# Kernel tuning notes

Measured on AMD Instinct MI355X. Metric: run time of the kernel, lower is better.

Reference implementation:

```python
import jax, jax.numpy as jnp
import numpy as np

B, D, H, W = 16, 96, 96, 96
NUM_POINTS = 4096
THRESH = 0.5
CH = [3, 64, 128, 256, 512]   # shared-MLP channel progression (3 mlp layers + global_dim)
GROUPS = 8
EPS = 1e-5
HEAD_HIDDEN = 128


def setup_inputs() -> dict:
    key = jax.random.key(0)
    ks = jax.random.split(key, 8)
    inp = {"volume": jax.random.uniform(ks[0], (B, 1, D, H, W), jnp.float32)}
    for i in range(4):
        # Conv1d(kernel=1, no bias) weight (out, in); kaiming normal fan_out -> std=sqrt(2/out)
        inp[f"w{i+1}"] = jax.random.normal(ks[1 + i], (CH[i + 1], CH[i]), jnp.float32) * np.sqrt(2.0 / CH[i + 1]).astype(np.float32)
        inp[f"gn{i+1}_w"] = jnp.ones((CH[i + 1],), jnp.float32)
        inp[f"gn{i+1}_b"] = jnp.zeros((CH[i + 1],), jnp.float32)
    inp["fc1_w"] = jax.random.normal(ks[5], (HEAD_HIDDEN, CH[-1]), jnp.float32) * np.sqrt(2.0 / HEAD_HIDDEN).astype(np.float32)
    inp["fc1_b"] = jnp.zeros((HEAD_HIDDEN,), jnp.float32)
    inp["fc2_w"] = jax.random.normal(ks[6], (1, HEAD_HIDDEN), jnp.float32) * np.sqrt(2.0).astype(np.float32)
    inp["fc2_b"] = jnp.zeros((1,), jnp.float32)
    return inp


def volume_to_points(volume):
    """Batched, jit-safe version of volume_to_pointcloud (eval mode: linspace sampling)."""
    b, _, d, h, w = volume.shape
    mask = (volume[:, 0] > THRESH).reshape(b, -1)              # (B, D*H*W)
    n = mask.sum(axis=1)                                        # (B,) foreground counts
    # Stable argsort on ~mask puts foreground flat-indices first, in ascending order
    # == torch nonzero() ordering (row-major over D,H,W).
    order = jnp.argsort(jnp.logical_not(mask), axis=1, stable=True)  # (B, D*H*W)
    p = jnp.arange(NUM_POINTS)
    n_f = n.astype(jnp.float32)[:, None]
    # torch.linspace(0, n-1, P).long(): truncation toward zero
    lin = (p[None, :].astype(jnp.float32) * (n_f - 1.0) / (NUM_POINTS - 1)).astype(jnp.int32)
    lin = jnp.clip(lin, 0, jnp.maximum(n[:, None] - 1, 0))
    wrap = p[None, :] % jnp.maximum(n[:, None], 1)              # n < P fallback
    idx = jnp.where(n[:, None] >= NUM_POINTS, lin, wrap)        # (B, P)
    flat = jnp.take_along_axis(order, idx, axis=1)              # (B, P) flat voxel indices
    dd = flat // (h * w)
    hh = (flat // w) % h
    ww = flat % w
    coords = jnp.stack([dd, hh, ww], axis=1).astype(jnp.float32)  # (B, 3, P)
    scale = jnp.array([max(d - 1, 1), max(h - 1, 1), max(w - 1, 1)], jnp.float32)
    pts = coords / scale[None, :, None] * 2.0 - 1.0
    return jnp.where((n > 0)[:, None, None], pts, 0.0)


def group_norm(x, gamma, beta):
    b, c, npts = x.shape
    xg = x.reshape(b, GROUPS, c // GROUPS, npts)
    mu = xg.mean(axis=(2, 3), keepdims=True)
    var = xg.var(axis=(2, 3), keepdims=True)
    xn = ((xg - mu) * jax.lax.rsqrt(var + EPS)).reshape(b, c, npts)
    return xn * gamma[None, :, None] + beta[None, :, None]


def reference(volume, w1, gn1_w, gn1_b, w2, gn2_w, gn2_b, w3, gn3_w, gn3_b,
              w4, gn4_w, gn4_b, fc1_w, fc1_b, fc2_w, fc2_b):
    x = volume_to_points(volume)                                 # (B, 3, P)
    for cw, gw, gb in ((w1, gn1_w, gn1_b), (w2, gn2_w, gn2_b),
                       (w3, gn3_w, gn3_b), (w4, gn4_w, gn4_b)):
        x = jax.nn.relu(group_norm(jnp.einsum('oc,bcn->bon', cw, x), gw, gb))
    g = x.max(axis=2)                                            # (B, 512) global max-pool
    hdn = jax.nn.relu(g @ fc1_w.T + fc1_b)                       # dropout is identity in eval
    logits = (hdn @ fc2_w.T + fc2_b)[:, 0]                       # squeeze(-1) -> (B,)
    return logits
```

## Files before the change

kernel.cpp:

```cpp
#include <hip/hip_runtime.h>
#include <hip/hip_bf16.h>

#define NB 16
#define VOX 884736
#define NPTS 4096
#define CHUNK 1024
#define NCHUNK 864

typedef _Float16 f16x8 __attribute__((ext_vector_type(8)));
typedef _Float16 f16x4 __attribute__((ext_vector_type(4)));
typedef float f32x4 __attribute__((ext_vector_type(4)));


__global__ __launch_bounds__(256) void count_kernel(const float* __restrict__ vol,
                                                    int* __restrict__ counts,
                                                    unsigned long long* __restrict__ bits) {
    int blk = blockIdx.x;
    const float4* v4 = (const float4*)(vol + (size_t)blk * CHUNK);
    float4 v = v4[threadIdx.x];
    int nib = (v.x > 0.5f) | ((v.y > 0.5f) << 1) | ((v.z > 0.5f) << 2) | ((v.w > 0.5f) << 3);
    __shared__ unsigned char nibs[256];
    nibs[threadIdx.x] = (unsigned char)nib;
    int cnt = __popc(nib);
    for (int off = 32; off; off >>= 1) cnt += __shfl_down(cnt, off, 64);
    __shared__ int s[4];
    if ((threadIdx.x & 63) == 0) s[threadIdx.x >> 6] = cnt;
    __syncthreads();
    if (threadIdx.x < 16) {
        unsigned long long wd = 0;
        #pragma unroll
        for (int i = 0; i < 16; i++)
            wd |= (unsigned long long)nibs[threadIdx.x * 16 + i] << (4 * i);
        bits[(size_t)blk * 16 + threadIdx.x] = wd;
    }
    if (threadIdx.x == 0) counts[blk] = s[0] + s[1] + s[2] + s[3];
}

__global__ __launch_bounds__(1024) void scan_kernel(const int* __restrict__ counts,
                                                    int* __restrict__ prefix,
                                                    int* __restrict__ totals) {
    __shared__ int s[1024];
    int b = blockIdx.x, t = threadIdx.x;
    int v = (t < NCHUNK) ? counts[b * NCHUNK + t] : 0;
    s[t] = v;
    __syncthreads();
    for (int off = 1; off < 1024; off <<= 1) {
        int x = (t >= off) ? s[t - off] : 0;
        __syncthreads();
        s[t] += x;
        __syncthreads();
    }
    if (t < NCHUNK) prefix[b * NCHUNK + t] = s[t] - v;
    if (t == NCHUNK - 1) totals[b] = s[t];
}


__global__ __launch_bounds__(256) void points_kernel(const unsigned long long* __restrict__ bits,
                                                     const int* __restrict__ prefix,
                                                     const int* __restrict__ totals,
                                                     const float* __restrict__ w1,
                                                     float* __restrict__ pts,
                                                     float* __restrict__ pstat1) {
    int b = blockIdx.x >> 4;
    int pc = blockIdx.x & 15;
    int p = pc * 256 + threadIdx.x;
    __shared__ int spref[NCHUNK];
    __shared__ float sw1[192];
    for (int i = threadIdx.x; i < NCHUNK; i += 256) spref[i] = prefix[b * NCHUNK + i];
    if (threadIdx.x < 192) sw1[threadIdx.x] = w1[threadIdx.x];
    __syncthreads();
    int n = totals[b];
    float px = 0.f, py = 0.f, pz = 0.f;
    if (n > 0) {
        int k;
        if (n >= NPTS) {
            float t = (float)p * ((float)n - 1.0f);
            t = t / 4095.0f;
            k = (int)t;
            if (k > n - 1) k = n - 1;
            if (k < 0) k = 0;
        } else {
            k = p % n;
        }
        int lo = 0, hi = NCHUNK - 1;
        while (lo < hi) {
            int mid = (lo + hi + 1) >> 1;
            if (spref[mid] <= k) lo = mid; else hi = mid - 1;
        }
        int rr = k - spref[lo];
        const unsigned long long* wb = bits + ((size_t)b * NCHUNK + lo) * 16;
        unsigned long long chosen = 0;
        int wordidx = 0;
        bool found = false;
        #pragma unroll
        for (int w = 0; w < 16; w++) {
            unsigned long long m = wb[w];
            int pcnt = __popcll(m);
            bool take = (!found) && (rr < pcnt);
            if (take) { chosen = m; wordidx = w; found = true; }
            if (!found) rr -= pcnt;
        }
        int pos = 0;
        unsigned long long m64 = chosen;
        int c = __popcll(m64 & 0xFFFFFFFFull);
        if (rr >= c) { pos = 32; rr -= c; m64 >>= 32; }
        unsigned mm = (unsigned)m64;
        c = __popc(mm & 0xFFFFu); if (rr >= c) { pos += 16; rr -= c; mm >>= 16; }
        c = __popc(mm & 0xFFu);   if (rr >= c) { pos += 8;  rr -= c; mm >>= 8; }
        c = __popc(mm & 0xFu);    if (rr >= c) { pos += 4;  rr -= c; mm >>= 4; }
        c = __popc(mm & 0x3u);    if (rr >= c) { pos += 2;  rr -= c; mm >>= 2; }
        c = mm & 1u;              if (rr >= c) { pos += 1; }
        int flat = lo * CHUNK + wordidx * 64 + pos;
        int dd = flat / 9216;
        int rem = flat - dd * 9216;
        int hh = rem / 96;
        int ww = rem - hh * 96;
        px = (float)dd / 95.0f * 2.0f - 1.0f;
        py = (float)hh / 95.0f * 2.0f - 1.0f;
        pz = (float)ww / 95.0f * 2.0f - 1.0f;
    }
    pts[((size_t)b * 3 + 0) * NPTS + p] = px;
    pts[((size_t)b * 3 + 1) * NPTS + p] = py;
    pts[((size_t)b * 3 + 2) * NPTS + p] = pz;
    float s[8] = {}, q[8] = {};
    #pragma unroll
    for (int o = 0; o < 64; o++) {
        float a = sw1[o * 3 + 0] * px + sw1[o * 3 + 1] * py + sw1[o * 3 + 2] * pz;
        s[o >> 3] += a;
        q[o >> 3] += a * a;
    }
    __shared__ float red[4][8][2];
    int wv = threadIdx.x >> 6;
    #pragma unroll
    for (int g = 0; g < 8; g++) {
        float S = s[g], Q = q[g];
        for (int off = 32; off; off >>= 1) {
            S += __shfl_down(S, off, 64);
            Q += __shfl_down(Q, off, 64);
        }
        if ((threadIdx.x & 63) == 0) { red[wv][g][0] = S; red[wv][g][1] = Q; }
    }
    __syncthreads();
    if (threadIdx.x < 8) {
        int g = threadIdx.x;
        float S = red[0][g][0] + red[1][g][0] + red[2][g][0] + red[3][g][0];
        float Q = red[0][g][1] + red[1][g][1] + red[2][g][1] + red[3][g][1];
        float* d = pstat1 + (((size_t)(b * 8 + g)) * 16 + pc) * 2;
        d[0] = S; d[1] = Q;
    }
}

__global__ __launch_bounds__(64) void gn_finalize1(const float* __restrict__ pstat,
                                                   const float* __restrict__ gamma,
                                                   const float* __restrict__ beta,
                                                   float* __restrict__ scale,
                                                   float* __restrict__ shift) {
    int b = blockIdx.x >> 3, g = blockIdx.x & 7;
    const float* base = pstat + (size_t)(b * 8 + g) * 32;
    float S = 0.f, Q = 0.f;
    if (threadIdx.x < 16) { S = base[threadIdx.x * 2]; Q = base[threadIdx.x * 2 + 1]; }
    for (int off = 8; off; off >>= 1) {
        S += __shfl_down(S, off, 64);
        Q += __shfl_down(Q, off, 64);
    }
    __shared__ float ms[2];
    if (threadIdx.x == 0) {
        float inv = 1.0f / (8.0f * 4096.0f);
        float mu = S * inv;
        float var = Q * inv - mu * mu;
        if (var < 0.f) var = 0.f;
        ms[0] = mu; ms[1] = rsqrtf(var + 1e-5f);
    }
    __syncthreads();
    if (threadIdx.x < 8) {
        int c = g * 8 + threadIdx.x;
        float ga = gamma[c] * ms[1];
        scale[b * 64 + c] = ga;
        shift[b * 64 + c] = beta[c] - ms[0] * ga;
    }
}


__device__ inline void cast_chunk(const float* __restrict__ wf, _Float16* __restrict__ wh,
                                  int CIN, int t) {
    int lane = t & 63;
    int NCB = CIN / 32;
    int cb = (t >> 6) % NCB;
    int ob = t / (64 * NCB);
    int o = ob * 16 + (lane & 15);
    int c0 = cb * 32 + (lane >> 4) * 8;
    const float* src = wf + (size_t)o * CIN + c0;
    f16x8 v;
    #pragma unroll
    for (int e = 0; e < 8; e++) v[e] = (_Float16)src[e];
    *(f16x8*)(wh + (size_t)t * 8) = v;
}

__global__ __launch_bounds__(256) void cast_w_all(const float* __restrict__ w2,
                                                  const float* __restrict__ w3,
                                                  const float* __restrict__ w4,
                                                  _Float16* __restrict__ w2f,
                                                  _Float16* __restrict__ w3f,
                                                  _Float16* __restrict__ w4f) {
    int t = blockIdx.x * 256 + threadIdx.x;
    if (t < 1024) cast_chunk(w2, w2f, 64, t);
    else if (t < 1024 + 4096) cast_chunk(w3, w3f, 128, t - 1024);
    else if (t < 1024 + 4096 + 16384) cast_chunk(w4, w4f, 256, t - 5120);
}


__global__ __launch_bounds__(256) void fused_l2(const float* __restrict__ pts,
                                                const float* __restrict__ w1,
                                                const float* __restrict__ scale,
                                                const float* __restrict__ shift,
                                                const _Float16* __restrict__ wfrag,
                                                _Float16* __restrict__ yout,
                                                float* __restrict__ pstat) {
    constexpr int CIN = 64, COUT = 128, NCB = 2;
    __shared__ char smem[8192];
    __shared__ float sw1[192], ssc[64], ssh[64];
    _Float16* sl = (_Float16*)smem;
    float* sred = (float*)smem;
    int b = blockIdx.y, pblk = blockIdx.x, tid = threadIdx.x;
    int Pg = b * 64 + pblk;
    if (tid < 192) sw1[tid] = w1[tid];
    if (tid < 64) { ssc[tid] = scale[b * 64 + tid]; ssh[tid] = shift[b * 64 + tid]; }
    __syncthreads();
    {
        int p = tid >> 2, qo = (tid & 3) * 16;
        int pg = pblk * 64 + p;
        float x0 = pts[((size_t)b * 3 + 0) * NPTS + pg];
        float x1 = pts[((size_t)b * 3 + 1) * NPTS + pg];
        float x2 = pts[((size_t)b * 3 + 2) * NPTS + pg];
        #pragma unroll
        for (int e = 0; e < 16; e++) {
            int o = qo + e;
            float a = sw1[o * 3 + 0] * x0 + sw1[o * 3 + 1] * x1 + sw1[o * 3 + 2] * x2;
            float r = fmaxf(a * ssc[o] + ssh[o], 0.f);
            int ch = o >> 3;
            sl[p * CIN + ((ch ^ (p & 7)) << 3) + (o & 7)] = (_Float16)r;
        }
    }
    __syncthreads();
    int wv = tid >> 6, lane = tid & 63, lr = lane & 15, lk = lane >> 4;
    int p = wv * 16 + lr;
    f16x8 af[NCB];
    #pragma unroll
    for (int cb = 0; cb < NCB; cb++) {
        int ch = cb * 4 + lk;
        af[cb] = *(const f16x8*)(sl + p * CIN + ((ch ^ (p & 7)) << 3));
    }
    __syncthreads();
    #pragma unroll 2
    for (int of = 0; of < COUT / 16; of++) {
        f32x4 acc = {};
        #pragma unroll
        for (int cb = 0; cb < NCB; cb++) {
            f16x8 bf = *(const f16x8*)(wfrag + ((size_t)(of * NCB + cb) * 64 + lane) * 8);
            acc = __builtin_amdgcn_mfma_f32_16x16x32_f16(af[cb], bf, acc, 0, 0, 0);
        }
        f16x4 vv;
        #pragma unroll
        for (int j = 0; j < 4; j++) vv[j] = (_Float16)acc[j];
        *(f16x4*)(yout + ((size_t)Pg * (COUT / 64) + (of >> 2)) * 4096 +
                  (((of & 3) * 4 + wv) * 64 + lane) * 4) = vv;
        float S = acc[0] + acc[1] + acc[2] + acc[3];
        float Q = acc[0] * acc[0] + acc[1] * acc[1] + acc[2] * acc[2] + acc[3] * acc[3];
        S += __shfl_xor(S, 16, 64); Q += __shfl_xor(Q, 16, 64);
        S += __shfl_xor(S, 32, 64); Q += __shfl_xor(Q, 32, 64);
        if (lk == 0) {
            float* d = sred + ((size_t)(wv * COUT + of * 16 + lr)) * 2;
            d[0] = S; d[1] = Q;
        }
    }
    __syncthreads();
    for (int o = tid; o < COUT; o += 256) {
        float S = 0.f, Q = 0.f;
        #pragma unroll
        for (int w = 0; w < 4; w++) {
            const float* d = sred + ((size_t)(w * COUT + o)) * 2;
            S += d[0]; Q += d[1];
        }
        float* d = pstat + (((size_t)(b * 64 + pblk)) * COUT + o) * 2;
        d[0] = S; d[1] = Q;
    }
}


template <int CIN, int COUT, bool POOL>
__global__ __launch_bounds__(256) void fused_layer(const _Float16* __restrict__ yprev,
                                                   const float* __restrict__ scale,
                                                   const float* __restrict__ shift,
                                                   const _Float16* __restrict__ wfrag,
                                                   _Float16* __restrict__ yout,
                                                   float* __restrict__ pstat) {
    constexpr int NCB = CIN / 32;
    constexpr int NST = POOL ? 4 : 2;
    constexpr int STAGE_B = 64 * CIN * 2;
    constexpr int SRED_B = 4 * COUT * NST * 4;
    constexpr int UNION_B = STAGE_B > SRED_B ? STAGE_B : SRED_B;
    __shared__ char smem[UNION_B];
    __shared__ float ssc[CIN], ssh[CIN];
    _Float16* sl = (_Float16*)smem;
    float* sred = (float*)smem;
    int b = blockIdx.y, pblk = blockIdx.x, tid = threadIdx.x;
    int Pg = b * 64 + pblk;
    for (int i = tid; i < CIN; i += 256) { ssc[i] = scale[b * CIN + i]; ssh[i] = shift[b * CIN + i]; }
    __syncthreads();
    const _Float16* yt = yprev + (size_t)Pg * 64 * CIN;
    constexpr int NCH4 = 64 * CIN / 4;
    for (int q = tid; q < NCH4; q += 256) {
        int lane = q & 63;
        int pf = (q >> 6) & 3;
        int ofi = (q >> 8) & 3;
        int Ob = q >> 10;
        int o = Ob * 64 + ofi * 16 + (lane & 15);
        int pbase = pf * 16 + (lane >> 4) * 4;
        f16x4 v = *(const f16x4*)(yt + (size_t)q * 4);
        float sc = ssc[o], sh = ssh[o];
        int ch = o >> 3;
        #pragma unroll
        for (int e = 0; e < 4; e++) {
            int p = pbase + e;
            float r = fmaxf((float)v[e] * sc + sh, 0.f);
            sl[p * CIN + ((ch ^ (p & 7)) << 3) + (o & 7)] = (_Float16)r;
        }
    }
    __syncthreads();
    int wv = tid >> 6, lane = tid & 63, lr = lane & 15, lk = lane >> 4;
    int p = wv * 16 + lr;
    f16x8 af[NCB];
    #pragma unroll
    for (int cb = 0; cb < NCB; cb++) {
        int ch = cb * 4 + lk;
        af[cb] = *(const f16x8*)(sl + p * CIN + ((ch ^ (p & 7)) << 3));
    }
    __syncthreads();
    #pragma unroll 2
    for (int of = 0; of < COUT / 16; of++) {
        f32x4 acc = {};
        #pragma unroll
        for (int cb = 0; cb < NCB; cb++) {
            f16x8 bf = *(const f16x8*)(wfrag + ((size_t)(of * NCB + cb) * 64 + lane) * 8);
            acc = __builtin_amdgcn_mfma_f32_16x16x32_f16(af[cb], bf, acc, 0, 0, 0);
        }
        if (!POOL) {
            f16x4 vv;
            #pragma unroll
            for (int j = 0; j < 4; j++) vv[j] = (_Float16)acc[j];
            *(f16x4*)(yout + ((size_t)Pg * (COUT / 64) + (of >> 2)) * 4096 +
                      (((of & 3) * 4 + wv) * 64 + lane) * 4) = vv;
        }
        float S = acc[0] + acc[1] + acc[2] + acc[3];
        float Q = acc[0] * acc[0] + acc[1] * acc[1] + acc[2] * acc[2] + acc[3] * acc[3];
        float MX = 0.f, MN = 0.f;
        if (POOL) {
            MX = fmaxf(fmaxf(acc[0], acc[1]), fmaxf(acc[2], acc[3]));
            MN = fminf(fminf(acc[0], acc[1]), fminf(acc[2], acc[3]));
        }
        S += __shfl_xor(S, 16, 64); Q += __shfl_xor(Q, 16, 64);
        S += __shfl_xor(S, 32, 64); Q += __shfl_xor(Q, 32, 64);
        if (POOL) {
            MX = fmaxf(MX, __shfl_xor(MX, 16, 64)); MN = fminf(MN, __shfl_xor(MN, 16, 64));
            MX = fmaxf(MX, __shfl_xor(MX, 32, 64)); MN = fminf(MN, __shfl_xor(MN, 32, 64));
        }
        if (lk == 0) {
            float* d = sred + ((size_t)(wv * COUT + of * 16 + lr)) * NST;
            d[0] = S; d[1] = Q;
            if (POOL) { d[2] = MX; d[3] = MN; }
        }
    }
    __syncthreads();
    for (int o = tid; o < COUT; o += 256) {
        float S = 0.f, Q = 0.f, MX = -1e30f, MN = 1e30f;
        #pragma unroll
        for (int w = 0; w < 4; w++) {
            const float* d = sred + ((size_t)(w * COUT + o)) * NST;
            S += d[0]; Q += d[1];
            if (POOL) { MX = fmaxf(MX, d[2]); MN = fminf(MN, d[3]); }
        }
        float* d = pstat + (((size_t)(b * 64 + pblk)) * COUT + o) * NST;
        if (POOL) *(float4*)d = make_float4(S, Q, MX, MN);
        else { d[0] = S; d[1] = Q; }
    }
}


template <int C>
__global__ __launch_bounds__(256) void gn_finalizeG(const float* __restrict__ pstat,
                                                    const float* __restrict__ gamma,
                                                    const float* __restrict__ beta,
                                                    float* __restrict__ scale,
                                                    float* __restrict__ shift) {
    constexpr int GS = C / 8;
    int b = blockIdx.x >> 3, g = blockIdx.x & 7;
    const float* base = pstat + (size_t)b * 64 * C * 2;
    float S = 0.f, Q = 0.f;
    for (int i = threadIdx.x; i < 64 * GS; i += 256) {
        int pb = i / GS;
        int c = g * GS + (i % GS);
        const float* d = base + ((size_t)pb * C + c) * 2;
        S += d[0]; Q += d[1];
    }
    for (int off = 32; off; off >>= 1) {
        S += __shfl_down(S, off, 64);
        Q += __shfl_down(Q, off, 64);
    }
    __shared__ float ss[8];
    if ((threadIdx.x & 63) == 0) {
        ss[(threadIdx.x >> 6) * 2] = S;
        ss[(threadIdx.x >> 6) * 2 + 1] = Q;
    }
    __syncthreads();
    __shared__ float ms[2];
    if (threadIdx.x == 0) {
        float St = ss[0] + ss[2] + ss[4] + ss[6];
        float Qt = ss[1] + ss[3] + ss[5] + ss[7];
        float inv = 1.0f / ((float)GS * 4096.0f);
        float mu = St * inv;
        float var = Qt * inv - mu * mu;
        if (var < 0.f) var = 0.f;
        ms[0] = mu; ms[1] = rsqrtf(var + 1e-5f);
    }
    __syncthreads();
    for (int i = threadIdx.x; i < GS; i += 256) {
        int c = g * GS + i;
        float ga = gamma[c] * ms[1];
        scale[(size_t)b * C + c] = ga;
        shift[(size_t)b * C + c] = beta[c] - ms[0] * ga;
    }
}


__global__ __launch_bounds__(256) void pool_final(const float* __restrict__ pstat4,
                                                  const float* __restrict__ gamma,
                                                  const float* __restrict__ beta,
                                                  float* __restrict__ g) {
    int b = blockIdx.x;
    __shared__ float sS[512], sQ[512];
    __shared__ float ms[8][2];
    float MXa[2], MNa[2];
    #pragma unroll
    for (int h = 0; h < 2; h++) {
        int o = threadIdx.x + h * 256;
        float S = 0.f, Q = 0.f, MX = -1e30f, MN = 1e30f;
        for (int pb = 0; pb < 64; pb++) {
            float4 v = *(const float4*)(pstat4 + (((size_t)(b * 64 + pb)) * 512 + o) * 4);
            S += v.x; Q += v.y; MX = fmaxf(MX, v.z); MN = fminf(MN, v.w);
        }
        MXa[h] = MX; MNa[h] = MN;
        sS[o] = S; sQ[o] = Q;
    }
    __syncthreads();
    if (threadIdx.x < 8) {
        int gr = threadIdx.x;
        float St = 0.f, Qt = 0.f;
        for (int i = 0; i < 64; i++) { St += sS[gr * 64 + i]; Qt += sQ[gr * 64 + i]; }
        float inv = 1.0f / (64.0f * 4096.0f);
        float mu = St * inv;
        float var = Qt * inv - mu * mu;
        if (var < 0.f) var = 0.f;
        ms[gr][0] = mu; ms[gr][1] = rsqrtf(var + 1e-5f);
    }
    __syncthreads();
    #pragma unroll
    for (int h = 0; h < 2; h++) {
        int o = threadIdx.x + h * 256;
        int gr = o >> 6;
        float sc = gamma[o] * ms[gr][1];
        float sh = beta[o] - ms[gr][0] * sc;
        float m = (sc >= 0.f ? MXa[h] : MNa[h]) * sc + sh;
        g[b * 512 + o] = fmaxf(m, 0.f);
    }
}


__global__ __launch_bounds__(128) void head_kernel(const float* __restrict__ g,
                                                   const float* __restrict__ fc1w,
                                                   const float* __restrict__ fc1b,
                                                   const float* __restrict__ fc2w,
                                                   const float* __restrict__ fc2b,
                                                   float* __restrict__ out) {
    int b = blockIdx.x;
    int o = threadIdx.x;
    __shared__ float sg[512];
    for (int i = threadIdx.x; i < 512; i += 128) sg[i] = g[b * 512 + i];
    __syncthreads();
    float acc = fc1b[o];
    for (int c = 0; c < 512; c++) acc += sg[c] * fc1w[o * 512 + c];
    float h = fmaxf(acc, 0.f) * fc2w[o];
    for (int off = 32; off; off >>= 1) h += __shfl_down(h, off, 64);
    __shared__ float s2[2];
    if ((threadIdx.x & 63) == 0) s2[threadIdx.x >> 6] = h;
    __syncthreads();
    if (threadIdx.x == 0) out[b] = s2[0] + s2[1] + fc2b[0];
}


extern "C" void kernel_launch(void* const* d_in, const int* in_sizes, int n_in,
                              void* d_out, int out_size, void* d_ws, size_t ws_size,
                              hipStream_t stream) {
    const float* vol  = (const float*)d_in[0];
    const float* w1   = (const float*)d_in[1];
    const float* gn1w = (const float*)d_in[2];
    const float* gn1b = (const float*)d_in[3];
    const float* w2   = (const float*)d_in[4];
    const float* gn2w = (const float*)d_in[5];
    const float* gn2b = (const float*)d_in[6];
    const float* w3   = (const float*)d_in[7];
    const float* gn3w = (const float*)d_in[8];
    const float* gn3b = (const float*)d_in[9];
    const float* w4   = (const float*)d_in[10];
    const float* gn4w = (const float*)d_in[11];
    const float* gn4b = (const float*)d_in[12];
    const float* fc1w = (const float*)d_in[13];
    const float* fc1b = (const float*)d_in[14];
    const float* fc2w = (const float*)d_in[15];
    const float* fc2b = (const float*)d_in[16];
    float* out = (float*)d_out;

    char* ws = (char*)d_ws;
    size_t cur = 0;
    auto alloc = [&](size_t bytes) -> void* {
        cur = (cur + 255) & ~(size_t)255;
        void* p = ws + cur;
        cur += bytes;
        return p;
    };
    int*      counts  = (int*)alloc((size_t)NB * NCHUNK * 4);
    int*      prefix  = (int*)alloc((size_t)NB * NCHUNK * 4);
    int*      totals  = (int*)alloc(64);
    unsigned long long* bits = (unsigned long long*)alloc((size_t)NB * NCHUNK * 16 * 8);
    float*    pts     = (float*)alloc((size_t)NB * 3 * NPTS * 4);
    float*    gbuf    = (float*)alloc((size_t)NB * 512 * 4);
    float*    pstat1  = (float*)alloc((size_t)NB * 8 * 16 * 2 * 4);
    float*    pstatG  = (float*)alloc((size_t)NB * 64 * 256 * 2 * 4);
    float*    pstat4  = (float*)alloc((size_t)NB * 64 * 512 * 4 * 4);
    float*    scale   = (float*)alloc((size_t)NB * 512 * 4);
    float*    shift   = (float*)alloc((size_t)NB * 512 * 4);
    _Float16* w2f     = (_Float16*)alloc((size_t)128 * 64 * 2);
    _Float16* w3f     = (_Float16*)alloc((size_t)256 * 128 * 2);
    _Float16* w4f     = (_Float16*)alloc((size_t)512 * 256 * 2);
    _Float16* y2      = (_Float16*)alloc((size_t)NB * NPTS * 128 * 2);
    _Float16* y3      = (_Float16*)alloc((size_t)NB * NPTS * 256 * 2);

    count_kernel<<<dim3(NB * NCHUNK), dim3(256), 0, stream>>>(vol, counts, bits);
    scan_kernel<<<dim3(NB), dim3(1024), 0, stream>>>(counts, prefix, totals);
    points_kernel<<<dim3(NB * 16), dim3(256), 0, stream>>>(bits, prefix, totals, w1, pts, pstat1);

    cast_w_all<<<dim3(84), dim3(256), 0, stream>>>(w2, w3, w4, w2f, w3f, w4f);

    gn_finalize1<<<dim3(NB * 8), dim3(64), 0, stream>>>(pstat1, gn1w, gn1b, scale, shift);
    fused_l2<<<dim3(64, NB), dim3(256), 0, stream>>>(pts, w1, scale, shift, w2f, y2, pstatG);

    gn_finalizeG<128><<<dim3(NB * 8), dim3(256), 0, stream>>>(pstatG, gn2w, gn2b, scale, shift);
    fused_layer<128, 256, false><<<dim3(64, NB), dim3(256), 0, stream>>>(y2, scale, shift, w3f, y3, pstatG);

    gn_finalizeG<256><<<dim3(NB * 8), dim3(256), 0, stream>>>(pstatG, gn3w, gn3b, scale, shift);
    fused_layer<256, 512, true><<<dim3(64, NB), dim3(256), 0, stream>>>(y3, scale, shift, w4f, nullptr, pstat4);

    pool_final<<<dim3(NB), dim3(256), 0, stream>>>(pstat4, gn4w, gn4b, gbuf);
    head_kernel<<<dim3(NB), dim3(128), 0, stream>>>(gbuf, fc1w, fc1b, fc2w, fc2b, out);
}
```

Baseline: 139.6 us.

## Split output channels across waves in MFMA GEMM and parallelize pool finalize

The per-layer GEMM is restructured so each wave covers all 64 points of the block and its own slice of output channels, up to four fragments at a time. Before, each wave owned 16 points and looped over every output channel. Each weight fragment loaded from global memory is now reused across four point fragments, and the cross-wave shared-memory reduction of statistics is removed because each wave writes complete per-channel stats. pool_final is also split into one 64-thread block per (batch, group), which raises parallelism and replaces the shared-memory reduction with wave shuffles. The trade-off is more accumulator registers per thread, which may lower occupancy.

```diff
diff --git a/kernel.cpp b/kernel.cpp
--- a/kernel.cpp
+++ b/kernel.cpp
@@ -209,6 +209,84 @@
 }
 
 
+template <int CIN, int COUT, bool POOL>
+__device__ __forceinline__ void gemm_core(const _Float16* __restrict__ sl,
+                                          const _Float16* __restrict__ wfrag,
+                                          _Float16* __restrict__ yout,
+                                          float* __restrict__ pstat,
+                                          int b, int pblk, int tid) {
+    constexpr int NCB = CIN / 32;
+    constexpr int OFW = COUT / 64;
+    constexpr int COF = OFW > 4 ? 4 : OFW;
+    constexpr int NCHK = OFW / COF;
+    int wv = tid >> 6, lane = tid & 63, lr = lane & 15, lk = lane >> 4;
+    int Pg = b * 64 + pblk;
+    #pragma unroll
+    for (int ck = 0; ck < NCHK; ck++) {
+        f32x4 acc[4][COF] = {};
+        #pragma unroll
+        for (int cb = 0; cb < NCB; cb++) {
+            f16x8 af[4];
+            int ch = cb * 4 + lk;
+            #pragma unroll
+            for (int pf = 0; pf < 4; pf++) {
+                int p = pf * 16 + lr;
+                af[pf] = *(const f16x8*)(sl + p * CIN + ((ch ^ (p & 7)) << 3));
+            }
+            f16x8 bf[COF];
+            #pragma unroll
+            for (int i = 0; i < COF; i++) {
+                int ofr = wv * OFW + ck * COF + i;
+                bf[i] = *(const f16x8*)(wfrag + ((size_t)(ofr * NCB + cb) * 64 + lane) * 8);
+            }
+            #pragma unroll
+            for (int pf = 0; pf < 4; pf++)
+                #pragma unroll
+                for (int i = 0; i < COF; i++)
+                    acc[pf][i] = __builtin_amdgcn_mfma_f32_16x16x32_f16(af[pf], bf[i], acc[pf][i], 0, 0, 0);
+        }
+        #pragma unroll
+        for (int i = 0; i < COF; i++) {
+            int ofr = wv * OFW + ck * COF + i;
+            if (!POOL) {
+                _Float16* ytO = yout + ((size_t)Pg * (COUT / 64) + (ofr >> 2)) * 4096;
+                #pragma unroll
+                for (int pf = 0; pf < 4; pf++) {
+                    f16x4 vv;
+                    #pragma unroll
+                    for (int j = 0; j < 4; j++) vv[j] = (_Float16)acc[pf][i][j];
+                    *(f16x4*)(ytO + (((ofr & 3) * 4 + pf) * 64 + lane) * 4) = vv;
+                }
+            }
+            float S = 0.f, Q = 0.f, MX = -1e30f, MN = 1e30f;
+            #pragma unroll
+            for (int pf = 0; pf < 4; pf++)
+                #pragma unroll
+                for (int j = 0; j < 4; j++) {
+                    float v = acc[pf][i][j];
+                    S += v; Q += v * v;
+                    if (POOL) { MX = fmaxf(MX, v); MN = fminf(MN, v); }
+                }
+            S += __shfl_xor(S, 16, 64); Q += __shfl_xor(Q, 16, 64);
+            S += __shfl_xor(S, 32, 64); Q += __shfl_xor(Q, 32, 64);
+            if (POOL) {
+                MX = fmaxf(MX, __shfl_xor(MX, 16, 64)); MN = fminf(MN, __shfl_xor(MN, 16, 64));
+                MX = fmaxf(MX, __shfl_xor(MX, 32, 64)); MN = fminf(MN, __shfl_xor(MN, 32, 64));
+            }
+            if (lk == 0) {
+                int o = ofr * 16 + lr;
+                if (POOL) {
+                    *(float4*)(pstat + ((size_t)Pg * COUT + o) * 4) = make_float4(S, Q, MX, MN);
+                } else {
+                    float* d = pstat + ((size_t)Pg * COUT + o) * 2;
+                    d[0] = S; d[1] = Q;
+                }
+            }
+        }
+    }
+}
+
+
 __global__ __launch_bounds__(256) void fused_l2(const float* __restrict__ pts,
                                                 const float* __restrict__ w1,
                                                 const float* __restrict__ scale,
@@ -216,13 +294,9 @@
                                                 const _Float16* __restrict__ wfrag,
                                                 _Float16* __restrict__ yout,
                                                 float* __restrict__ pstat) {
-    constexpr int CIN = 64, COUT = 128, NCB = 2;
-    __shared__ char smem[8192];
+    __shared__ _Float16 sl[64 * 64];
     __shared__ float sw1[192], ssc[64], ssh[64];
-    _Float16* sl = (_Float16*)smem;
-    float* sred = (float*)smem;
     int b = blockIdx.y, pblk = blockIdx.x, tid = threadIdx.x;
-    int Pg = b * 64 + pblk;
     if (tid < 192) sw1[tid] = w1[tid];
     if (tid < 64) { ssc[tid] = scale[b * 64 + tid]; ssh[tid] = shift[b * 64 + tid]; }
     __syncthreads();
@@ -237,53 +311,11 @@
             int o = qo + e;
             float a = sw1[o * 3 + 0] * x0 + sw1[o * 3 + 1] * x1 + sw1[o * 3 + 2] * x2;
             float r = fmaxf(a * ssc[o] + ssh[o], 0.f);
-            int ch = o >> 3;
-            sl[p * CIN + ((ch ^ (p & 7)) << 3) + (o & 7)] = (_Float16)r;
-        }
-    }
-    __syncthreads();
-    int wv = tid >> 6, lane = tid & 63, lr = lane & 15, lk = lane >> 4;
-    int p = wv * 16 + lr;
-    f16x8 af[NCB];
-    #pragma unroll
-    for (int cb = 0; cb < NCB; cb++) {
-        int ch = cb * 4 + lk;
-        af[cb] = *(const f16x8*)(sl + p * CIN + ((ch ^ (p & 7)) << 3));
-    }
-    __syncthreads();
-    #pragma unroll 2
-    for (int of = 0; of < COUT / 16; of++) {
-        f32x4 acc = {};
-        #pragma unroll
-        for (int cb = 0; cb < NCB; cb++) {
-            f16x8 bf = *(const f16x8*)(wfrag + ((size_t)(of * NCB + cb) * 64 + lane) * 8);
-            acc = __builtin_amdgcn_mfma_f32_16x16x32_f16(af[cb], bf, acc, 0, 0, 0);
-        }
-        f16x4 vv;
-        #pragma unroll
-        for (int j = 0; j < 4; j++) vv[j] = (_Float16)acc[j];
-        *(f16x4*)(yout + ((size_t)Pg * (COUT / 64) + (of >> 2)) * 4096 +
-                  (((of & 3) * 4 + wv) * 64 + lane) * 4) = vv;
-        float S = acc[0] + acc[1] + acc[2] + acc[3];
-        float Q = acc[0] * acc[0] + acc[1] * acc[1] + acc[2] * acc[2] + acc[3] * acc[3];
-        S += __shfl_xor(S, 16, 64); Q += __shfl_xor(Q, 16, 64);
-        S += __shfl_xor(S, 32, 64); Q += __shfl_xor(Q, 32, 64);
-        if (lk == 0) {
-            float* d = sred + ((size_t)(wv * COUT + of * 16 + lr)) * 2;
-            d[0] = S; d[1] = Q;
-        }
-    }
-    __syncthreads();
-    for (int o = tid; o < COUT; o += 256) {
-        float S = 0.f, Q = 0.f;
-        #pragma unroll
-        for (int w = 0; w < 4; w++) {
-            const float* d = sred + ((size_t)(w * COUT + o)) * 2;
-            S += d[0]; Q += d[1];
-        }
-        float* d = pstat + (((size_t)(b * 64 + pblk)) * COUT + o) * 2;
-        d[0] = S; d[1] = Q;
-    }
+            sl[p * 64 + (((o >> 3) ^ (p & 7)) << 3) + (o & 7)] = (_Float16)r;
+        }
+    }
+    __syncthreads();
+    gemm_core<64, 128, false>(sl, wfrag, yout, pstat, b, pblk, tid);
 }
 
 
@@ -294,15 +326,8 @@
                                                    const _Float16* __restrict__ wfrag,
                                                    _Float16* __restrict__ yout,
                                                    float* __restrict__ pstat) {
-    constexpr int NCB = CIN / 32;
-    constexpr int NST = POOL ? 4 : 2;
-    constexpr int STAGE_B = 64 * CIN * 2;
-    constexpr int SRED_B = 4 * COUT * NST * 4;
-    constexpr int UNION_B = STAGE_B > SRED_B ? STAGE_B : SRED_B;
-    __shared__ char smem[UNION_B];
+    __shared__ _Float16 sl[64 * CIN];
     __shared__ float ssc[CIN], ssh[CIN];
-    _Float16* sl = (_Float16*)smem;
-    float* sred = (float*)smem;
     int b = blockIdx.y, pblk = blockIdx.x, tid = threadIdx.x;
     int Pg = b * 64 + pblk;
     for (int i = tid; i < CIN; i += 256) { ssc[i] = scale[b * CIN + i]; ssh[i] = shift[b * CIN + i]; }
@@ -327,62 +352,7 @@
         }
     }
     __syncthreads();
-    int wv = tid >> 6, lane = tid & 63, lr = lane & 15, lk = lane >> 4;
-    int p = wv * 16 + lr;
-    f16x8 af[NCB];
-    #pragma unroll
-    for (int cb = 0; cb < NCB; cb++) {
-        int ch = cb * 4 + lk;
-        af[cb] = *(const f16x8*)(sl + p * CIN + ((ch ^ (p & 7)) << 3));
-    }
-    __syncthreads();
-    #pragma unroll 2
-    for (int of = 0; of < COUT / 16; of++) {
-        f32x4 acc = {};
-        #pragma unroll
-        for (int cb = 0; cb < NCB; cb++) {
-            f16x8 bf = *(const f16x8*)(wfrag + ((size_t)(of * NCB + cb) * 64 + lane) * 8);
-            acc = __builtin_amdgcn_mfma_f32_16x16x32_f16(af[cb], bf, acc, 0, 0, 0);
-        }
-        if (!POOL) {
-            f16x4 vv;
-            #pragma unroll
-            for (int j = 0; j < 4; j++) vv[j] = (_Float16)acc[j];
-            *(f16x4*)(yout + ((size_t)Pg * (COUT / 64) + (of >> 2)) * 4096 +
-                      (((of & 3) * 4 + wv) * 64 + lane) * 4) = vv;
-        }
-        float S = acc[0] + acc[1] + acc[2] + acc[3];
-        float Q = acc[0] * acc[0] + acc[1] * acc[1] + acc[2] * acc[2] + acc[3] * acc[3];
-        float MX = 0.f, MN = 0.f;
-        if (POOL) {
-            MX = fmaxf(fmaxf(acc[0], acc[1]), fmaxf(acc[2], acc[3]));
-            MN = fminf(fminf(acc[0], acc[1]), fminf(acc[2], acc[3]));
-        }
-        S += __shfl_xor(S, 16, 64); Q += __shfl_xor(Q, 16, 64);
-        S += __shfl_xor(S, 32, 64); Q += __shfl_xor(Q, 32, 64);
-        if (POOL) {
-            MX = fmaxf(MX, __shfl_xor(MX, 16, 64)); MN = fminf(MN, __shfl_xor(MN, 16, 64));
-            MX = fmaxf(MX, __shfl_xor(MX, 32, 64)); MN = fminf(MN, __shfl_xor(MN, 32, 64));
-        }
-        if (lk == 0) {
-            float* d = sred + ((size_t)(wv * COUT + of * 16 + lr)) * NST;
-            d[0] = S; d[1] = Q;
-            if (POOL) { d[2] = MX; d[3] = MN; }
-        }
-    }
-    __syncthreads();
-    for (int o = tid; o < COUT; o += 256) {
-        float S = 0.f, Q = 0.f, MX = -1e30f, MN = 1e30f;
-        #pragma unroll
-        for (int w = 0; w < 4; w++) {
-            const float* d = sred + ((size_t)(w * COUT + o)) * NST;
-            S += d[0]; Q += d[1];
-            if (POOL) { MX = fmaxf(MX, d[2]); MN = fminf(MN, d[3]); }
-        }
-        float* d = pstat + (((size_t)(b * 64 + pblk)) * COUT + o) * NST;
-        if (POOL) *(float4*)d = make_float4(S, Q, MX, MN);
-        else { d[0] = S; d[1] = Q; }
-    }
+    gemm_core<CIN, COUT, POOL>(sl, wfrag, yout, pstat, b, pblk, tid);
 }
 
 
@@ -432,46 +402,31 @@
 }
 
 
-__global__ __launch_bounds__(256) void pool_final(const float* __restrict__ pstat4,
-                                                  const float* __restrict__ gamma,
-                                                  const float* __restrict__ beta,
-                                                  float* __restrict__ g) {
-    int b = blockIdx.x;
-    __shared__ float sS[512], sQ[512];
-    __shared__ float ms[8][2];
-    float MXa[2], MNa[2];
-    #pragma unroll
-    for (int h = 0; h < 2; h++) {
-        int o = threadIdx.x + h * 256;
-        float S = 0.f, Q = 0.f, MX = -1e30f, MN = 1e30f;
-        for (int pb = 0; pb < 64; pb++) {
-            float4 v = *(const float4*)(pstat4 + (((size_t)(b * 64 + pb)) * 512 + o) * 4);
-            S += v.x; Q += v.y; MX = fmaxf(MX, v.z); MN = fminf(MN, v.w);
-        }
-        MXa[h] = MX; MNa[h] = MN;
-        sS[o] = S; sQ[o] = Q;
-    }
-    __syncthreads();
-    if (threadIdx.x < 8) {
-        int gr = threadIdx.x;
-        float St = 0.f, Qt = 0.f;
-        for (int i = 0; i < 64; i++) { St += sS[gr * 64 + i]; Qt += sQ[gr * 64 + i]; }
-        float inv = 1.0f / (64.0f * 4096.0f);
-        float mu = St * inv;
-        float var = Qt * inv - mu * mu;
-        if (var < 0.f) var = 0.f;
-        ms[gr][0] = mu; ms[gr][1] = rsqrtf(var + 1e-5f);
-    }
-    __syncthreads();
-    #pragma unroll
-    for (int h = 0; h < 2; h++) {
-        int o = threadIdx.x + h * 256;
-        int gr = o >> 6;
-        float sc = gamma[o] * ms[gr][1];
-        float sh = beta[o] - ms[gr][0] * sc;
-        float m = (sc >= 0.f ? MXa[h] : MNa[h]) * sc + sh;
-        g[b * 512 + o] = fmaxf(m, 0.f);
-    }
+__global__ __launch_bounds__(64) void pool_final(const float* __restrict__ pstat4,
+                                                 const float* __restrict__ gamma,
+                                                 const float* __restrict__ beta,
+                                                 float* __restrict__ g) {
+    int b = blockIdx.x >> 3, gr = blockIdx.x & 7;
+    int o = gr * 64 + threadIdx.x;
+    float S = 0.f, Q = 0.f, MX = -1e30f, MN = 1e30f;
+    for (int pb = 0; pb < 64; pb++) {
+        float4 v = *(const float4*)(pstat4 + (((size_t)(b * 64 + pb)) * 512 + o) * 4);
+        S += v.x; Q += v.y; MX = fmaxf(MX, v.z); MN = fminf(MN, v.w);
+    }
+    float St = S, Qt = Q;
+    for (int off = 32; off; off >>= 1) {
+        St += __shfl_xor(St, off, 64);
+        Qt += __shfl_xor(Qt, off, 64);
+    }
+    float inv = 1.0f / (64.0f * 4096.0f);
+    float mu = St * inv;
+    float var = Qt * inv - mu * mu;
+    if (var < 0.f) var = 0.f;
+    float rstd = rsqrtf(var + 1e-5f);
+    float sc = gamma[o] * rstd;
+    float sh = beta[o] - mu * sc;
+    float m = (sc >= 0.f ? MX : MN) * sc + sh;
+    g[b * 512 + o] = fmaxf(m, 0.f);
 }
 
 
@@ -559,6 +514,6 @@
     gn_finalizeG<256><<<dim3(NB * 8), dim3(256), 0, stream>>>(pstatG, gn3w, gn3b, scale, shift);
     fused_layer<256, 512, true><<<dim3(64, NB), dim3(256), 0, stream>>>(y3, scale, shift, w4f, nullptr, pstat4);
 
-    pool_final<<<dim3(NB), dim3(256), 0, stream>>>(pstat4, gn4w, gn4b, gbuf);
+    pool_final<<<dim3(NB * 8), dim3(64), 0, stream>>>(pstat4, gn4w, gn4b, gbuf);
     head_kernel<<<dim3(NB), dim3(128), 0, stream>>>(gbuf, fc1w, fc1b, fc2w, fc2b, out);
 }
```

After: 126.0 us. 9.7% less time.
